# Kernel optimization log

Measured on AMD Instinct MI355X. Metric: run time of the kernel, lower is better.

## Reference

```python
import jax, jax.numpy as jnp
import numpy as np

EPS = 1e-5      # BatchNorm eps (eval mode, running stats at init: mean=0, var=1)
SLOPE = 0.2     # LeakyReLU negative slope


def _knn_idx(x, k):
    # x: (B, N, D) -> (B, N, k) indices of k nearest neighbors (squared L2, feature space)
    sq = jnp.sum(x * x, axis=-1)                              # (B, N)
    dist = sq[:, :, None] + sq[:, None, :] - 2.0 * jnp.einsum('bnd,bmd->bnm', x, x)
    return jax.lax.top_k(-dist, k)[1]                         # nearest = largest of -dist


def _bn_lrelu(y, gamma, beta):
    # eval BatchNorm with running_mean=0, running_var=1, then LeakyReLU(0.2)
    y = y * (gamma / jnp.sqrt(1.0 + EPS)) + beta
    return jnp.where(y >= 0, y, SLOPE * y)


def _edge_conv(x, W, gamma, beta, k):
    # x: (B, N, D); W: (C_out, 2D). Returns (B, N, C_out) after max over k neighbors.
    idx = _knn_idx(x, k)                                      # (B, N, k)
    nb = jax.vmap(lambda xt, i: xt[i])(x, idx)                # (B, N, k, D) neighbor gather
    ctr = jnp.broadcast_to(x[:, :, None, :], nb.shape)
    feat = jnp.concatenate([nb - ctr, ctr], axis=-1)          # (B, N, k, 2D)
    y = jnp.einsum('bnkd,od->bnko', feat, W)                  # 1x1 conv (no bias)
    y = _bn_lrelu(y, gamma, beta)
    return jnp.max(y, axis=2)                                 # max-pool over neighbors


def setup_inputs() -> dict:
    key = jax.random.key(0)
    ks = jax.random.split(key, 16)
    B, N, k, out_dim = 8, 4096, 20, 512
    x = jax.random.normal(ks[0], (B, 3, N), dtype=jnp.float32)
    dims = [(64, 6), (64, 128), (128, 128), (256, 256), (out_dim, 512)]
    inp = {'x': x, 'k': k}
    for i, (co, ci) in enumerate(dims, start=1):
        inp[f'W{i}'] = jax.random.normal(ks[3 * i - 2], (co, ci), dtype=jnp.float32) * (1.0 / np.sqrt(ci))
        inp[f'g{i}'] = jax.random.uniform(ks[3 * i - 1], (co,), dtype=jnp.float32, minval=0.5, maxval=1.5)
        inp[f'b{i}'] = 0.1 * jax.random.normal(ks[3 * i], (co,), dtype=jnp.float32)
    return inp


def reference(x, W1, g1, b1, W2, g2, b2, W3, g3, b3, W4, g4, b4, W5, g5, b5, k):
    xt = jnp.transpose(x, (0, 2, 1))                          # (B, N, 3)
    x1 = _edge_conv(xt, W1, g1, b1, k)                        # (B, N, 64)
    x2 = _edge_conv(x1, W2, g2, b2, k)                        # (B, N, 64)
    x3 = _edge_conv(x2, W3, g3, b3, k)                        # (B, N, 128)
    x4 = _edge_conv(x3, W4, g4, b4, k)                        # (B, N, 256)
    h = jnp.concatenate([x1, x2, x3, x4], axis=-1)            # (B, N, 512)
    y = _bn_lrelu(jnp.einsum('bnd,od->bno', h, W5), g5, b5)   # (B, N, out_dim)
    return jnp.concatenate([jnp.max(y, axis=1), jnp.mean(y, axis=1)], axis=-1)  # (B, 2*out_dim)
```

## Files before the change

### kernel.cpp

```cpp
#include <hip/hip_runtime.h>
#include <math.h>

#define BATCH 8
#define N_PTS 4096
#define KNN 20
#define EPS_BN 1e-5f
#define SLOPE 0.2f
#define M_ROWS (BATCH * N_PTS)

typedef __attribute__((ext_vector_type(8))) short short8;
typedef __attribute__((ext_vector_type(4))) float float4v;
typedef __attribute__((ext_vector_type(16))) float float16v;

__device__ __forceinline__ unsigned short f2bf(float f) {
    unsigned u = __float_as_uint(f);
    unsigned r = (u + 0x7FFFu + ((u >> 16) & 1u)) >> 16;
    return (unsigned short)r;
}
__device__ __forceinline__ float bf2f(unsigned short h) {
    return __uint_as_float((unsigned)h << 16);
}

__global__ void convert_x1(const float* __restrict__ x,
                           unsigned short* __restrict__ xh, unsigned short* __restrict__ xl,
                           float* __restrict__ sq) {
    int i = blockIdx.x * blockDim.x + threadIdx.x;
    if (i >= M_ROWS) return;
    int b = i / N_PTS, n = i % N_PTS;
    float v[3], s = 0.f;
    #pragma unroll
    for (int d = 0; d < 3; ++d) {
        v[d] = x[((size_t)b * 3 + d) * N_PTS + n];
        s += v[d] * v[d];
    }
    sq[i] = s;
    #pragma unroll
    for (int d = 0; d < 32; ++d) {
        float f = (d < 3) ? v[d] : 0.f;
        unsigned short h = f2bf(f);
        xh[(size_t)i * 32 + d] = h;
        xl[(size_t)i * 32 + d] = f2bf(f - bf2f(h));
    }
}

__global__ void sqnorm_hl(const unsigned short* __restrict__ hh,
                          const unsigned short* __restrict__ hl,
                          int D, float* __restrict__ sq) {
    int w = threadIdx.x >> 6, lane = threadIdx.x & 63;
    int row = blockIdx.x * 4 + w;
    if (row >= M_ROWS) return;
    const unsigned short* ph = hh + (size_t)row * 512;
    const unsigned short* pl = hl + (size_t)row * 512;
    float s = 0.f;
    for (int d = lane; d < D; d += 64) {
        float v = bf2f(ph[d]) + bf2f(pl[d]);
        s += v * v;
    }
    #pragma unroll
    for (int off = 32; off > 0; off >>= 1) s += __shfl_down(s, off, 64);
    if (lane == 0) sq[row] = s;
}

__global__ void repack_edge_split(const float* __restrict__ W, int Co, int D, int KP,
                                  unsigned short* __restrict__ Wh, unsigned short* __restrict__ Wl) {
    int i = blockIdx.x * blockDim.x + threadIdx.x;
    int tot = 2 * Co * KP;
    if (i >= tot) return;
    int r = i / KP, d = i % KP;
    float v = 0.f;
    if (d < D) v = (r < Co) ? W[(size_t)r * 2 * D + d] : W[(size_t)(r - Co) * 2 * D + D + d];
    unsigned short h = f2bf(v);
    Wh[i] = h; Wl[i] = f2bf(v - bf2f(h));
}

__global__ void repack_w5_split(const float* __restrict__ W,
                                unsigned short* __restrict__ Wh, unsigned short* __restrict__ Wl) {
    int i = blockIdx.x * blockDim.x + threadIdx.x;
    if (i >= 512 * 512) return;
    float v = W[i];
    unsigned short h = f2bf(v);
    Wh[i] = h; Wl[i] = f2bf(v - bf2f(h));
}

template<int DPAD>
__launch_bounds__(256, 2)
__global__ void knn_mfma(const unsigned short* __restrict__ Xh,
                         const unsigned short* __restrict__ Xl,
                         int strideX,
                         const float* __restrict__ sq, int* __restrict__ idxout) {
    constexpr int KS16 = DPAD / 16;
    constexpr int C8   = DPAD / 8;
    constexpr int XK   = (C8 - 1) < 7 ? (C8 - 1) : 7;
    constexpr int SB   = 64 * DPAD;
    constexpr size_t STAGE = (size_t)2 * SB * 2 + (size_t)64 * 65 * 4 + 64 * 4;
    constexpr size_t MERGE = (size_t)64 * 61 * 4 * 2;
    constexpr size_t POOL  = STAGE > MERGE ? STAGE : MERGE;
    __shared__ __align__(16) char smem[POOL];
    unsigned short* BhS = (unsigned short*)smem;
    unsigned short* BlS = BhS + SB;
    float* Sf  = (float*)(smem + (size_t)2 * SB * 2);
    float* sqs = Sf + 64 * 65;
    float*    kb = (float*)smem;
    unsigned* ib = (unsigned*)(kb + 64 * 61);

    const int b = blockIdx.y;
    const int row0 = blockIdx.x * 64;
    const int tid = threadIdx.x;
    const int w = tid >> 6, lane = tid & 63;
    const int l31 = lane & 31, lh = lane >> 5;
    const int r = tid & 63, t = tid >> 6;
    const int rbase = (w & 1) * 32;
    const int cb32  = (w >> 1) * 32;

    const unsigned short* Xhb = Xh + (size_t)b * N_PTS * strideX;
    const unsigned short* Xlb = Xl + (size_t)b * N_PTS * strideX;
    const float* sqb = sq + (size_t)b * N_PTS;

    short8 ah[KS16], al[KS16];
    #pragma unroll
    for (int ks = 0; ks < KS16; ++ks) {
        size_t o = (size_t)(row0 + rbase + l31) * strideX + ks * 16 + lh * 8;
        ah[ks] = *(const short8*)(Xhb + o);
        al[ks] = *(const short8*)(Xlb + o);
    }

    float fv[KNN]; int fi[KNN];
    #pragma unroll
    for (int p = 0; p < KNN; ++p) { fv[p] = INFINITY; fi[p] = 0x7FFFFFFF; }

    for (int c0 = 0; c0 < N_PTS; c0 += 64) {
        __syncthreads();
        #pragma unroll
        for (int it = 0; it < (64 * C8 + 255) / 256; ++it) {
            int tt = tid + it * 256;
            int col = tt / C8, kcs = tt % C8;
            int kcg = kcs ^ (col & XK);
            size_t o = (size_t)(c0 + col) * strideX + kcg * 8;
            *(short8*)&BhS[tt * 8] = *(const short8*)(Xhb + o);
            *(short8*)&BlS[tt * 8] = *(const short8*)(Xlb + o);
        }
        if (tid < 64) sqs[tid] = sqb[c0 + tid];
        __syncthreads();

        float16v acc = {};

        const int colL = cb32 + l31;
        const int cbase_us = colL * DPAD;
        #pragma unroll
        for (int ks = 0; ks < KS16; ++ks) {
            int ch = ((ks * 2 + lh) ^ (colL & XK)) * 8;
            short8 bh = *(const short8*)&BhS[cbase_us + ch];
            short8 bl = *(const short8*)&BlS[cbase_us + ch];
            acc = __builtin_amdgcn_mfma_f32_32x32x16_bf16(ah[ks], bh, acc, 0, 0, 0);
            acc = __builtin_amdgcn_mfma_f32_32x32x16_bf16(al[ks], bh, acc, 0, 0, 0);
            acc = __builtin_amdgcn_mfma_f32_32x32x16_bf16(ah[ks], bl, acc, 0, 0, 0);
        }

        {
            float sc = sqs[colL];
            int pos = (colL & 3) * 16 + (colL >> 2);
            #pragma unroll
            for (int reg = 0; reg < 16; ++reg) {
                int rowL = rbase + (reg & 3) + 8 * (reg >> 2) + 4 * lh;
                Sf[rowL * 65 + pos] = sc - 2.f * acc[reg];
            }
        }
        __syncthreads();

        const int sbase = r * 65 + t * 16;
        unsigned mask = 0;
        #pragma unroll
        for (int jj = 0; jj < 16; ++jj) {
            float v = Sf[sbase + jj];
            if (v < fv[KNN - 1]) mask |= (1u << jj);
        }
        while (mask) {
            int jj = __ffs(mask) - 1;
            mask &= mask - 1;
            float v = Sf[sbase + jj];
            if (v < fv[KNN - 1]) {
                fv[KNN - 1] = v;
                fi[KNN - 1] = c0 + (jj << 2) + t;
                #pragma unroll
                for (int p = KNN - 1; p > 0; --p) {
                    float va = fv[p - 1], vb = fv[p];
                    int   ia = fi[p - 1], ic = fi[p];
                    bool sw = vb < va;
                    fv[p - 1] = sw ? vb : va; fv[p] = sw ? va : vb;
                    fi[p - 1] = sw ? ic : ia; fi[p] = sw ? ia : ic;
                }
            }
        }
    }
    __syncthreads();

    if (t > 0) {
        #pragma unroll
        for (int p = 0; p < KNN; ++p) {
            kb[r * 61 + (t - 1) * KNN + p] = fv[p];
            ib[r * 61 + (t - 1) * KNN + p] = (unsigned)fi[p];
        }
    }
    __syncthreads();
    if (tid < 64) {
        #pragma unroll 1
        for (int qq = 0; qq < 3 * KNN; ++qq) {
            float    v  = kb[tid * 61 + qq];
            unsigned ii = ib[tid * 61 + qq];
            bool ins = (v < fv[KNN - 1]) ||
                       (v == fv[KNN - 1] && (int)ii < fi[KNN - 1]);
            if (ins) {
                fv[KNN - 1] = v; fi[KNN - 1] = (int)ii;
                #pragma unroll
                for (int p = KNN - 1; p > 0; --p) {
                    float va = fv[p - 1], vb = fv[p];
                    int   ia = fi[p - 1], ic = fi[p];
                    bool sw = (vb < va) || (vb == va && ic < ia);
                    fv[p - 1] = sw ? vb : va; fv[p] = sw ? va : vb;
                    fi[p - 1] = sw ? ic : ia; fi[p] = sw ? ia : ic;
                }
            }
        }
        int* op = idxout + ((size_t)(b * N_PTS + row0 + tid)) * KNN;
        #pragma unroll
        for (int p = 0; p < KNN; ++p) op[p] = fi[p];
    }
}

__launch_bounds__(256)
__global__ void fgemm(const unsigned short* __restrict__ Ah, const unsigned short* __restrict__ Al,
                      int strideA, int K,
                      const unsigned short* __restrict__ Wh, const unsigned short* __restrict__ Wl,
                      int C, float* __restrict__ out, int fuse_bn,
                      const float* __restrict__ g, const float* __restrict__ beta) {
    __shared__ unsigned short AhS[128 * 40];
    __shared__ unsigned short AlS[128 * 40];
    __shared__ unsigned short BhS[128 * 40];
    __shared__ unsigned short BlS[128 * 40];

    const int c0 = blockIdx.x * 128;
    const int m0 = blockIdx.y * 128;
    const int tid = threadIdx.x;
    const int w = tid >> 6, lane = tid & 63;
    const int n = lane & 15, q = lane >> 4;

    float4v acc[2][8];
    #pragma unroll
    for (int rt = 0; rt < 2; ++rt)
        #pragma unroll
        for (int ct = 0; ct < 8; ++ct) acc[rt][ct] = (float4v){0.f, 0.f, 0.f, 0.f};

    for (int kk = 0; kk < K; kk += 32) {
        __syncthreads();
        for (int tt = tid; tt < 512; tt += 256) {
            int rr = tt >> 2, c8 = tt & 3;
            size_t oa = (size_t)(m0 + rr) * strideA + kk + c8 * 8;
            *(short8*)&AhS[rr * 40 + c8 * 8] = *(const short8*)(Ah + oa);
            *(short8*)&AlS[rr * 40 + c8 * 8] = *(const short8*)(Al + oa);
            size_t ob = (size_t)(c0 + rr) * K + kk + c8 * 8;
            *(short8*)&BhS[rr * 40 + c8 * 8] = *(const short8*)(Wh + ob);
            *(short8*)&BlS[rr * 40 + c8 * 8] = *(const short8*)(Wl + ob);
        }
        __syncthreads();

        short8 af[2][2];
        #pragma unroll
        for (int rt = 0; rt < 2; ++rt) {
            af[rt][0] = *(const short8*)&AhS[(w * 32 + rt * 16 + n) * 40 + q * 8];
            af[rt][1] = *(const short8*)&AlS[(w * 32 + rt * 16 + n) * 40 + q * 8];
        }
        #pragma unroll
        for (int ct = 0; ct < 8; ++ct) {
            short8 bh = *(const short8*)&BhS[(ct * 16 + n) * 40 + q * 8];
            short8 bl = *(const short8*)&BlS[(ct * 16 + n) * 40 + q * 8];
            #pragma unroll
            for (int rt = 0; rt < 2; ++rt) {
                acc[rt][ct] = __builtin_amdgcn_mfma_f32_16x16x32_bf16(af[rt][0], bh, acc[rt][ct], 0, 0, 0);
                acc[rt][ct] = __builtin_amdgcn_mfma_f32_16x16x32_bf16(af[rt][1], bh, acc[rt][ct], 0, 0, 0);
                acc[rt][ct] = __builtin_amdgcn_mfma_f32_16x16x32_bf16(af[rt][0], bl, acc[rt][ct], 0, 0, 0);
            }
        }
    }

    #pragma unroll
    for (int rt = 0; rt < 2; ++rt)
        #pragma unroll
        for (int ct = 0; ct < 8; ++ct) {
            int c = c0 + ct * 16 + n;
            float sc = 1.f, bt = 0.f;
            if (fuse_bn) { sc = g[c] / sqrtf(1.f + EPS_BN); bt = beta[c]; }
            #pragma unroll
            for (int e = 0; e < 4; ++e) {
                int m = m0 + w * 32 + rt * 16 + q * 4 + e;
                float v = acc[rt][ct][e];
                if (fuse_bn) { v = v * sc + bt; v = (v >= 0.f) ? v : SLOPE * v; }
                out[(size_t)m * C + c] = v;
            }
        }
}

__global__ void pool_kernel(const float* __restrict__ zc2, int Co,
                            const int* __restrict__ idx,
                            const float* __restrict__ g, const float* __restrict__ beta,
                            unsigned short* __restrict__ hh, unsigned short* __restrict__ hl,
                            int hoff) {
    int n = blockIdx.x, b = blockIdx.y;
    int o = threadIdx.x;
    size_t bn = (size_t)b * N_PTS + n;
    const int* ip = idx + bn * KNN;
    float zn   = zc2[bn * (size_t)(2 * Co) + o];
    float base = zc2[bn * (size_t)(2 * Co) + Co + o] - zn;
    float m = -INFINITY;
    #pragma unroll
    for (int j = 0; j < KNN; ++j) {
        size_t rr = (size_t)b * N_PTS + ip[j];
        m = fmaxf(m, zc2[rr * (size_t)(2 * Co) + o]);
    }
    float y = m + base;
    float sc = g[o] / sqrtf(1.f + EPS_BN);
    y = y * sc + beta[o];
    y = (y >= 0.f) ? y : SLOPE * y;
    unsigned short h = f2bf(y);
    hh[bn * 512 + hoff + o] = h;
    hl[bn * 512 + hoff + o] = f2bf(y - bf2f(h));
}

__global__ void reduce_partial(const float* __restrict__ y5,
                               float* __restrict__ pmax, float* __restrict__ psum) {
    int chunk = blockIdx.x, b = blockIdx.y, c = threadIdx.x;
    float mx = -INFINITY, sm = 0.f;
    for (int qq = 0; qq < 128; ++qq) {
        int n = chunk * 128 + qq;
        float v = y5[((size_t)b * N_PTS + n) * 512 + c];
        mx = fmaxf(mx, v);
        sm += v;
    }
    pmax[((size_t)b * 32 + chunk) * 512 + c] = mx;
    psum[((size_t)b * 32 + chunk) * 512 + c] = sm;
}

__global__ void reduce_final(const float* __restrict__ pmax,
                             const float* __restrict__ psum,
                             float* __restrict__ out) {
    int i = blockIdx.x * blockDim.x + threadIdx.x;
    if (i >= BATCH * 512) return;
    int b = i / 512, c = i % 512;
    float mx = -INFINITY, sm = 0.f;
    for (int qq = 0; qq < 32; ++qq) {
        mx = fmaxf(mx, pmax[((size_t)b * 32 + qq) * 512 + c]);
        sm += psum[((size_t)b * 32 + qq) * 512 + c];
    }
    out[(size_t)b * 1024 + c] = mx;
    out[(size_t)b * 1024 + 512 + c] = sm * (1.f / 4096.f);
}

extern "C" void kernel_launch(void* const* d_in, const int* in_sizes, int n_in,
                              void* d_out, int out_size, void* d_ws, size_t ws_size,
                              hipStream_t stream) {
    const float* x = (const float*)d_in[0];
    const float* W[5], *gg[5], *bb[5];
    for (int i = 0; i < 5; ++i) {
        W[i]  = (const float*)d_in[2 + 3 * i];
        gg[i] = (const float*)d_in[3 + 3 * i];
        bb[i] = (const float*)d_in[4 + 3 * i];
    }
    float* outp = (float*)d_out;

    char* wsb = (char*)d_ws;
    size_t off = 0;
    unsigned short* x1h = (unsigned short*)(wsb + off); off += (size_t)M_ROWS * 32 * 2;
    unsigned short* x1l = (unsigned short*)(wsb + off); off += (size_t)M_ROWS * 32 * 2;
    float* sq = (float*)(wsb + off); off += (size_t)M_ROWS * 4;
    int*   idx = (int*)(wsb + off); off += (size_t)M_ROWS * KNN * 4;
    unsigned short* Wh = (unsigned short*)(wsb + off); off += (size_t)512 * 512 * 2;
    unsigned short* Wl = (unsigned short*)(wsb + off); off += (size_t)512 * 512 * 2;
    unsigned short* hh = (unsigned short*)(wsb + off); off += (size_t)M_ROWS * 512 * 2;
    unsigned short* hl = (unsigned short*)(wsb + off); off += (size_t)M_ROWS * 512 * 2;
    float* zc2 = (float*)(wsb + off); off += (size_t)M_ROWS * 512 * 4;
    float* pmx = (float*)(wsb + off); off += (size_t)BATCH * 32 * 512 * 4;
    float* psm = (float*)(wsb + off); off += (size_t)BATCH * 32 * 512 * 4;
    (void)ws_size; (void)in_sizes; (void)n_in; (void)out_size;

    convert_x1<<<(M_ROWS + 255) / 256, 256, 0, stream>>>(x, x1h, x1l, sq);

    struct L { int D, Co, KP, hoff; };
    const L layers[4] = { {3, 64, 32, 0}, {64, 64, 64, 64}, {64, 128, 64, 128}, {128, 256, 128, 256} };

    for (int li = 0; li < 4; ++li) {
        const L& ly = layers[li];
        const unsigned short* Ahp;
        const unsigned short* Alp;
        int strideA;
        if (li == 0) { Ahp = x1h; Alp = x1l; strideA = 32; }
        else {
            int po = layers[li - 1].hoff;
            Ahp = hh + po; Alp = hl + po; strideA = 512;
            sqnorm_hl<<<M_ROWS / 4, 256, 0, stream>>>(Ahp, Alp, ly.D, sq);
        }

        if (li == 0)
            knn_mfma<32><<<dim3(N_PTS / 64, BATCH), 256, 0, stream>>>(Ahp, Alp, strideA, sq, idx);
        else if (ly.D == 64)
            knn_mfma<64><<<dim3(N_PTS / 64, BATCH), 256, 0, stream>>>(Ahp, Alp, strideA, sq, idx);
        else
            knn_mfma<128><<<dim3(N_PTS / 64, BATCH), 256, 0, stream>>>(Ahp, Alp, strideA, sq, idx);

        repack_edge_split<<<(2 * ly.Co * ly.KP + 255) / 256, 256, 0, stream>>>(
            W[li], ly.Co, ly.D, ly.KP, Wh, Wl);
        fgemm<<<dim3((2 * ly.Co) / 128, M_ROWS / 128), 256, 0, stream>>>(
            Ahp, Alp, strideA, ly.KP, Wh, Wl, 2 * ly.Co, zc2, 0, nullptr, nullptr);
        pool_kernel<<<dim3(N_PTS, BATCH), ly.Co, 0, stream>>>(
            zc2, ly.Co, idx, gg[li], bb[li], hh, hl, ly.hoff);
    }

    repack_w5_split<<<(512 * 512 + 255) / 256, 256, 0, stream>>>(W[4], Wh, Wl);
    fgemm<<<dim3(4, M_ROWS / 128), 256, 0, stream>>>(
        hh, hl, 512, 512, Wh, Wl, 512, zc2, 1, gg[4], bb[4]);

    reduce_partial<<<dim3(32, BATCH), 512, 0, stream>>>(zc2, pmx, psm);
    reduce_final<<<(BATCH * 512 + 255) / 256, 256, 0, stream>>>(pmx, psm, outp);
}
```

Measured before the change: 1.459 ms.

## Restructure kNN kernel to keep distances in registers and drop LDS staging

Rewrites the MFMA kNN kernel so each lane keeps its own top-k list for one query (the MFMA B operand) and candidate columns are loaded straight from global memory into registers, with no LDS tile staging. Per-column squared norms are preloaded to LDS once, and the per-tile __syncthreads and LDS score transpose are removed. Four partial lists per query are merged at the end instead of the previous arrangement. The intent is to cut barrier and LDS traffic per 64-column tile. In exchange, every wave now issues redundant global loads for candidate columns, and the final merge handles more lists.

```diff
diff --git a/kernel.cpp b/kernel.cpp
--- a/kernel.cpp
+++ b/kernel.cpp
@@ -88,99 +88,85 @@
                          const unsigned short* __restrict__ Xl,
                          int strideX,
                          const float* __restrict__ sq, int* __restrict__ idxout) {
-    constexpr int KS16 = DPAD / 16;
-    constexpr int C8   = DPAD / 8;
-    constexpr int XK   = (C8 - 1) < 7 ? (C8 - 1) : 7;
-    constexpr int SB   = 64 * DPAD;
-    constexpr size_t STAGE = (size_t)2 * SB * 2 + (size_t)64 * 65 * 4 + 64 * 4;
-    constexpr size_t MERGE = (size_t)64 * 61 * 4 * 2;
-    constexpr size_t POOL  = STAGE > MERGE ? STAGE : MERGE;
+    constexpr int KS = DPAD / 16;
+    constexpr size_t MAIN  = (size_t)4096 * 4 + (size_t)256 * 17 * 4;
+    constexpr size_t MERGE = (size_t)64 * 4 * KNN * 8;
+    constexpr size_t POOL  = MAIN > MERGE ? MAIN : MERGE;
     __shared__ __align__(16) char smem[POOL];
-    unsigned short* BhS = (unsigned short*)smem;
-    unsigned short* BlS = BhS + SB;
-    float* Sf  = (float*)(smem + (size_t)2 * SB * 2);
-    float* sqs = Sf + 64 * 65;
+    float* sqs = (float*)smem;
+    float* scr = sqs + 4096;
     float*    kb = (float*)smem;
-    unsigned* ib = (unsigned*)(kb + 64 * 61);
+    unsigned* ib = (unsigned*)(kb + 64 * 4 * KNN);
 
     const int b = blockIdx.y;
     const int row0 = blockIdx.x * 64;
     const int tid = threadIdx.x;
     const int w = tid >> 6, lane = tid & 63;
     const int l31 = lane & 31, lh = lane >> 5;
-    const int r = tid & 63, t = tid >> 6;
-    const int rbase = (w & 1) * 32;
-    const int cb32  = (w >> 1) * 32;
+    const int qg = w & 1, cg = w >> 1;
 
     const unsigned short* Xhb = Xh + (size_t)b * N_PTS * strideX;
     const unsigned short* Xlb = Xl + (size_t)b * N_PTS * strideX;
     const float* sqb = sq + (size_t)b * N_PTS;
 
-    short8 ah[KS16], al[KS16];
-    #pragma unroll
-    for (int ks = 0; ks < KS16; ++ks) {
-        size_t o = (size_t)(row0 + rbase + l31) * strideX + ks * 16 + lh * 8;
-        ah[ks] = *(const short8*)(Xhb + o);
-        al[ks] = *(const short8*)(Xlb + o);
+    {
+        const float4v* s4 = (const float4v*)sqb;
+        float4v* d4 = (float4v*)sqs;
+        #pragma unroll
+        for (int it = 0; it < 4; ++it) d4[tid + it * 256] = s4[tid + it * 256];
+    }
+    __syncthreads();
+
+    short8 qh[KS], ql[KS];
+    {
+        size_t qo = (size_t)(row0 + qg * 32 + l31) * strideX + lh * 8;
+        #pragma unroll
+        for (int ks = 0; ks < KS; ++ks) {
+            qh[ks] = *(const short8*)(Xhb + qo + ks * 16);
+            ql[ks] = *(const short8*)(Xlb + qo + ks * 16);
+        }
     }
 
     float fv[KNN]; int fi[KNN];
     #pragma unroll
     for (int p = 0; p < KNN; ++p) { fv[p] = INFINITY; fi[p] = 0x7FFFFFFF; }
 
+    const int scrb = tid * 17;
+
+    #pragma unroll 1
     for (int c0 = 0; c0 < N_PTS; c0 += 64) {
-        __syncthreads();
-        #pragma unroll
-        for (int it = 0; it < (64 * C8 + 255) / 256; ++it) {
-            int tt = tid + it * 256;
-            int col = tt / C8, kcs = tt % C8;
-            int kcg = kcs ^ (col & XK);
-            size_t o = (size_t)(c0 + col) * strideX + kcg * 8;
-            *(short8*)&BhS[tt * 8] = *(const short8*)(Xhb + o);
-            *(short8*)&BlS[tt * 8] = *(const short8*)(Xlb + o);
-        }
-        if (tid < 64) sqs[tid] = sqb[c0 + tid];
-        __syncthreads();
+        const int cbase = c0 + cg * 32;
+        short8 ch[KS], cl[KS];
+        size_t ro = (size_t)(cbase + l31) * strideX + lh * 8;
+        #pragma unroll
+        for (int ks = 0; ks < KS; ++ks) {
+            ch[ks] = *(const short8*)(Xhb + ro + ks * 16);
+            cl[ks] = *(const short8*)(Xlb + ro + ks * 16);
+        }
 
         float16v acc = {};
-
-        const int colL = cb32 + l31;
-        const int cbase_us = colL * DPAD;
-        #pragma unroll
-        for (int ks = 0; ks < KS16; ++ks) {
-            int ch = ((ks * 2 + lh) ^ (colL & XK)) * 8;
-            short8 bh = *(const short8*)&BhS[cbase_us + ch];
-            short8 bl = *(const short8*)&BlS[cbase_us + ch];
-            acc = __builtin_amdgcn_mfma_f32_32x32x16_bf16(ah[ks], bh, acc, 0, 0, 0);
-            acc = __builtin_amdgcn_mfma_f32_32x32x16_bf16(al[ks], bh, acc, 0, 0, 0);
-            acc = __builtin_amdgcn_mfma_f32_32x32x16_bf16(ah[ks], bl, acc, 0, 0, 0);
-        }
-
-        {
-            float sc = sqs[colL];
-            int pos = (colL & 3) * 16 + (colL >> 2);
-            #pragma unroll
-            for (int reg = 0; reg < 16; ++reg) {
-                int rowL = rbase + (reg & 3) + 8 * (reg >> 2) + 4 * lh;
-                Sf[rowL * 65 + pos] = sc - 2.f * acc[reg];
-            }
-        }
-        __syncthreads();
-
-        const int sbase = r * 65 + t * 16;
+        #pragma unroll
+        for (int ks = 0; ks < KS; ++ks) {
+            acc = __builtin_amdgcn_mfma_f32_32x32x16_bf16(ch[ks], qh[ks], acc, 0, 0, 0);
+            acc = __builtin_amdgcn_mfma_f32_32x32x16_bf16(cl[ks], qh[ks], acc, 0, 0, 0);
+            acc = __builtin_amdgcn_mfma_f32_32x32x16_bf16(ch[ks], ql[ks], acc, 0, 0, 0);
+        }
+
         unsigned mask = 0;
         #pragma unroll
-        for (int jj = 0; jj < 16; ++jj) {
-            float v = Sf[sbase + jj];
-            if (v < fv[KNN - 1]) mask |= (1u << jj);
+        for (int reg = 0; reg < 16; ++reg) {
+            int crow = (reg & 3) + 8 * (reg >> 2) + 4 * lh;
+            float v = fmaf(-2.f, acc[reg], sqs[cbase + crow]);
+            scr[scrb + reg] = v;
+            if (v < fv[KNN - 1]) mask |= (1u << reg);
         }
         while (mask) {
             int jj = __ffs(mask) - 1;
             mask &= mask - 1;
-            float v = Sf[sbase + jj];
+            float v = scr[scrb + jj];
             if (v < fv[KNN - 1]) {
                 fv[KNN - 1] = v;
-                fi[KNN - 1] = c0 + (jj << 2) + t;
+                fi[KNN - 1] = cbase + (jj & 3) + 8 * (jj >> 2) + 4 * lh;
                 #pragma unroll
                 for (int p = KNN - 1; p > 0; --p) {
                     float va = fv[p - 1], vb = fv[p];
@@ -194,23 +180,26 @@
     }
     __syncthreads();
 
-    if (t > 0) {
-        #pragma unroll
-        for (int p = 0; p < KNN; ++p) {
-            kb[r * 61 + (t - 1) * KNN + p] = fv[p];
-            ib[r * 61 + (t - 1) * KNN + p] = (unsigned)fi[p];
-        }
+    {
+        int qloc = qg * 32 + l31;
+        int list = cg * 2 + lh;
+        int base = (qloc * 4 + list) * KNN;
+        #pragma unroll
+        for (int p = 0; p < KNN; ++p) { kb[base + p] = fv[p]; ib[base + p] = (unsigned)fi[p]; }
     }
     __syncthreads();
+
     if (tid < 64) {
+        int base = tid * 4 * KNN;
+        #pragma unroll
+        for (int p = 0; p < KNN; ++p) { fv[p] = kb[base + p]; fi[p] = (int)ib[base + p]; }
         #pragma unroll 1
-        for (int qq = 0; qq < 3 * KNN; ++qq) {
-            float    v  = kb[tid * 61 + qq];
-            unsigned ii = ib[tid * 61 + qq];
-            bool ins = (v < fv[KNN - 1]) ||
-                       (v == fv[KNN - 1] && (int)ii < fi[KNN - 1]);
+        for (int qq = KNN; qq < 4 * KNN; ++qq) {
+            float    v  = kb[base + qq];
+            int      ii = (int)ib[base + qq];
+            bool ins = (v < fv[KNN - 1]) || (v == fv[KNN - 1] && ii < fi[KNN - 1]);
             if (ins) {
-                fv[KNN - 1] = v; fi[KNN - 1] = (int)ii;
+                fv[KNN - 1] = v; fi[KNN - 1] = ii;
                 #pragma unroll
                 for (int p = KNN - 1; p > 0; --p) {
                     float va = fv[p - 1], vb = fv[p];
```

New measurement: 1.467 ms. No clear change (+0.5%).
